# Kernel tuning notes

Measured on AMD Instinct MI355X. Metric: run time of the kernel, lower is better.

The kernel has to match this reference:

```python
import jax, jax.numpy as jnp
import numpy as np

EPS = 1e-5  # BatchNorm eps (torch default)

def _bn(x, mean, var, gamma, beta):
    # eval-mode BatchNorm over the trailing (heads, ch) axes
    return (x - mean) * (gamma / jnp.sqrt(var + EPS)) + beta

def setup_inputs() -> dict:
    key = jax.random.key(0)
    ks = jax.random.split(key, 8)
    B, C, W, H = 16, 256, 64, 64
    heads, k, u, m = 4, 16, 1, 23
    vv = 256
    kh, vh = k // heads, vv // heads
    x = jax.random.normal(ks[0], (B, C, W, H), dtype=jnp.float32)
    q_w = jax.random.normal(ks[1], (heads, kh, C), dtype=jnp.float32) * 0.05
    k_w = jax.random.normal(ks[2], (heads, kh * u, C), dtype=jnp.float32) * 0.05
    v_w = jax.random.normal(ks[3], (heads, vh * u, C), dtype=jnp.float32) * 0.05
    q_gamma = 0.5 + jax.random.uniform(ks[4], (heads, kh), dtype=jnp.float32)
    q_beta = jax.random.normal(ks[5], (heads, kh), dtype=jnp.float32) * 0.1
    q_mean = jnp.zeros((heads, kh), dtype=jnp.float32)
    q_var = jnp.ones((heads, kh), dtype=jnp.float32)
    k_gamma = 0.5 + jax.random.uniform(ks[6], (heads, kh * u), dtype=jnp.float32)
    k_beta = jax.random.normal(ks[7], (heads, kh * u), dtype=jnp.float32) * 0.1
    k_mean = jnp.zeros((heads, kh * u), dtype=jnp.float32)
    k_var = jnp.ones((heads, kh * u), dtype=jnp.float32)
    embedding = jax.random.normal(jax.random.fold_in(key, 99), (kh, heads, u, 1, m, m), dtype=jnp.float32) * 0.05
    return {"x": x, "q_w": q_w, "q_gamma": q_gamma, "q_beta": q_beta, "q_mean": q_mean,
            "q_var": q_var, "k_w": k_w, "k_gamma": k_gamma, "k_beta": k_beta,
            "k_mean": k_mean, "k_var": k_var, "v_w": v_w, "embedding": embedding}

def reference(x, q_w, q_gamma, q_beta, q_mean, q_var, k_w, k_gamma, k_beta, k_mean, k_var, v_w, embedding):
    B, C, W, H = x.shape
    heads, kh, _ = q_w.shape
    u = embedding.shape[2]
    m = embedding.shape[-1]
    vh = v_w.shape[1] // u
    pad = (m - 1) // 2

    # 1x1 conv projections (all heads stacked) -> channels-last
    q = jnp.einsum('bcxy,hkc->bxyhk', x, q_w)                      # [B,W,H,heads,kh]
    q = _bn(q, q_mean, q_var, q_gamma, q_beta)
    kk = jnp.einsum('bcxy,hkc->bxyhk', x, k_w)                     # [B,W,H,heads,kh*u]
    kk = _bn(kk, k_mean, k_var, k_gamma, k_beta)
    # softmax over all spatial positions, per (head, key-channel)
    sm = jax.nn.softmax(kk.reshape(B, W * H, heads, kh * u), axis=1)
    sm = sm.reshape(B, W, H, heads, kh, u)                          # [B,W,H,h,kh,u]
    v = jnp.einsum('bcxy,hvc->bxyhv', x, v_w).reshape(B, W, H, heads, vh, u)

    # content lambda: sum over all spatial positions
    lambda_c = jnp.einsum('bxyhku,bxyhvu->bhkv', sm, v)             # [B,h,kh,vh]
    y_c = jnp.einsum('bxyhk,bhkv->bxyhv', q, lambda_c)              # [B,W,H,h,vh]

    # positional lambda via grouped 2D conv (conv3d kernel depth is 1 -> 2D conv per vh slice)
    v_conv = v.transpose(0, 4, 3, 5, 1, 2).reshape(B * vh, heads * u, W, H)
    w = jnp.squeeze(embedding, axis=3).transpose(1, 0, 2, 3, 4).reshape(heads * kh, u, m, m)
    conv = jax.lax.conv_general_dilated(
        v_conv, w, window_strides=(1, 1), padding=[(pad, pad), (pad, pad)],
        dimension_numbers=('NCHW', 'OIHW', 'NCHW'), feature_group_count=heads)
    # [B*vh, heads*kh, W, H] -> sum over spatial (matches .sum(dim=[1,2]) in source)
    lambda_p = conv.reshape(B, vh, heads, kh, W, H).sum(axis=(4, 5))
    lambda_p = lambda_p.transpose(0, 2, 3, 1)                       # [B,h,kh,vh]
    y_p = jnp.einsum('bxyhk,bhkv->bxyhv', q, lambda_p)

    out = (y_c + y_p).reshape(B, W, H, heads * vh).transpose(0, 3, 1, 2)  # [B,vv,W,H]
    return out
```

## Files before the change

### kernel.cpp

```cpp
#include <hip/hip_runtime.h>
#include <math.h>

#define C_   256
#define WH   4096

typedef _Float16 f16x8 __attribute__((ext_vector_type(8)));
typedef float    f32x4 __attribute__((ext_vector_type(4)));


__global__ __launch_bounds__(256) void wtcomb_kernel(const float* __restrict__ emb,
                                                     const float* __restrict__ pstats,
                                                     float* __restrict__ Wt,
                                                     float* __restrict__ stats)
{
    if (blockIdx.x == 64) {
        int row = threadIdx.x;
        const float* ps = pstats + (size_t)row * 32;
        float M = ps[0];
#pragma unroll
        for (int ch = 1; ch < 16; ++ch) M = fmaxf(M, ps[ch * 2]);
        float S = 0.f;
#pragma unroll
        for (int ch = 0; ch < 16; ++ch) S += ps[ch * 2 + 1] * __expf(ps[ch * 2] - M);
        stats[row * 2 + 0] = M;
        stats[row * 2 + 1] = 1.f / S;
        return;
    }
    int hk = blockIdx.x >> 2, quarter = blockIdx.x & 3;
    int h = hk >> 2, k = hk & 3;
    const float* e = emb + (size_t)(k * 4 + h) * 529;
    __shared__ float colsum[23][64];
    for (int t = threadIdx.x; t < 23 * 64; t += 256) {
        int i = t / 64, q = t % 64;
        int jlo = max(0, q - 52), jhi = min(22, q + 11);
        float s = 0.f;
        for (int j = jlo; j <= jhi; ++j) s += e[i * 23 + j];
        colsum[i][q] = s;
    }
    __syncthreads();
    for (int tt = threadIdx.x; tt < 1024; tt += 256) {
        int t = quarter * 1024 + tt;
        int p = t >> 6, q = t & 63;
        int ilo = max(0, p - 52), ihi = min(22, p + 11);
        float s = 0.f;
        for (int i = ilo; i <= ihi; ++i) s += colsum[i][q];
        Wt[(size_t)hk * WH + t] = s;
    }
}

__global__ __launch_bounds__(512) void proj_kernel(
    const float* __restrict__ x,
    const float* __restrict__ qw, const float* __restrict__ kw,
    const float* __restrict__ qg, const float* __restrict__ qb,
    const float* __restrict__ qm, const float* __restrict__ qv,
    const float* __restrict__ kg, const float* __restrict__ kb,
    const float* __restrict__ km, const float* __restrict__ kv,
    float* __restrict__ qbn, float* __restrict__ kkbn, float* __restrict__ pstats)
{
    int t = threadIdx.x;
    int b = blockIdx.x >> 4, chunk = blockIdx.x & 15;
    int lane = t & 63;
    int og = __builtin_amdgcn_readfirstlane(t >> 6);
    int isK = og >> 2;
    int o4 = (og & 3) * 4;
    int xy = chunk * 256 + lane * 4;

    const float* wsrc = isK ? kw : qw;
    const float* w0 = wsrc + (size_t)(o4 + 0) * 256;
    const float* w1 = wsrc + (size_t)(o4 + 1) * 256;
    const float* w2 = wsrc + (size_t)(o4 + 2) * 256;
    const float* w3 = wsrc + (size_t)(o4 + 3) * 256;

    float4 a0 = {0,0,0,0}, a1 = {0,0,0,0}, a2 = {0,0,0,0}, a3 = {0,0,0,0};
    const float* xb = x + (size_t)b * C_ * WH + xy;
#pragma unroll 8
    for (int c = 0; c < 256; ++c) {
        float4 xv = *(const float4*)(xb + (size_t)c * WH);
        float f0 = w0[c], f1 = w1[c], f2 = w2[c], f3 = w3[c];
        a0.x += xv.x*f0; a0.y += xv.y*f0; a0.z += xv.z*f0; a0.w += xv.w*f0;
        a1.x += xv.x*f1; a1.y += xv.y*f1; a1.z += xv.z*f1; a1.w += xv.w*f1;
        a2.x += xv.x*f2; a2.y += xv.y*f2; a2.z += xv.z*f2; a2.w += xv.w*f2;
        a3.x += xv.x*f3; a3.y += xv.y*f3; a3.z += xv.z*f3; a3.w += xv.w*f3;
    }
    float4 acc4[4] = {a0, a1, a2, a3};

    if (!isK) {
#pragma unroll
        for (int i = 0; i < 4; ++i) {
            int hk = o4 + i;
            float s  = qg[hk] * rsqrtf(qv[hk] + 1e-5f);
            float tq = qb[hk] - qm[hk] * s;
            float4 a = acc4[i], o;
            o.x = a.x * s + tq; o.y = a.y * s + tq;
            o.z = a.z * s + tq; o.w = a.w * s + tq;
            *(float4*)(qbn + ((size_t)b * 16 + hk) * WH + xy) = o;
        }
    } else {
#pragma unroll
        for (int i = 0; i < 4; ++i) {
            int hk = o4 + i;
            float s2 = kg[hk] * rsqrtf(kv[hk] + 1e-5f);
            float tk = kb[hk] - km[hk] * s2;
            float4 a = acc4[i], o;
            o.x = a.x * s2 + tk; o.y = a.y * s2 + tk;
            o.z = a.z * s2 + tk; o.w = a.w * s2 + tk;
            *(float4*)(kkbn + ((size_t)b * 16 + hk) * WH + xy) = o;
            float m = fmaxf(fmaxf(o.x, o.y), fmaxf(o.z, o.w));
#pragma unroll
            for (int off = 32; off; off >>= 1) m = fmaxf(m, __shfl_xor(m, off, 64));
            float e = __expf(o.x - m) + __expf(o.y - m) + __expf(o.z - m) + __expf(o.w - m);
#pragma unroll
            for (int off = 32; off; off >>= 1) e += __shfl_xor(e, off, 64);
            if (lane == 0) {
                float* ps = pstats + ((size_t)(b * 16 + hk) * 16 + chunk) * 2;
                ps[0] = m; ps[1] = e;
            }
        }
    }
}

__global__ __launch_bounds__(512) void ut_kernel(
    const float* __restrict__ x, const float* __restrict__ kkbn,
    const float* __restrict__ stats, const float* __restrict__ Wt,
    float* __restrict__ Mpart)
{
    __shared__ _Float16 xls[256][72];
    __shared__ _Float16 wls[32][72];
    int t = threadIdx.x;
    int b = blockIdx.x >> 4, seg = blockIdx.x & 15;
    int xys0 = seg * 256;
    int lane = t & 63;
    int wid = __builtin_amdgcn_readfirstlane(t >> 6);
    int r16 = lane & 15, g = lane >> 4;
    int n0 = wid * 32;

    int sc = t >> 1, shalf = t & 1;
    int wr = t >> 3, wco = (t & 7) * 8;
    float wm = 0.f, winv = 0.f;
    if (t < 256 && wr < 16) {
        wm   = stats[(b * 16 + wr) * 2 + 0];
        winv = stats[(b * 16 + wr) * 2 + 1];
    }

    f32x4 acc00 = {0.f,0.f,0.f,0.f}, acc01 = {0.f,0.f,0.f,0.f};
    f32x4 acc10 = {0.f,0.f,0.f,0.f}, acc11 = {0.f,0.f,0.f,0.f};

    for (int ch = 0; ch < 4; ++ch) {
        int kbase = xys0 + ch * 64;
        __syncthreads();
        {
            const float* xp = x + ((size_t)b * C_ + sc) * WH + kbase + shalf * 32;
#pragma unroll
            for (int j = 0; j < 4; ++j) {
                float4 u  = *(const float4*)(xp + j * 8);
                float4 u2 = *(const float4*)(xp + j * 8 + 4);
                f16x8 o;
                o[0] = (_Float16)u.x;  o[1] = (_Float16)u.y;
                o[2] = (_Float16)u.z;  o[3] = (_Float16)u.w;
                o[4] = (_Float16)u2.x; o[5] = (_Float16)u2.y;
                o[6] = (_Float16)u2.z; o[7] = (_Float16)u2.w;
                *(f16x8*)&xls[sc][shalf * 32 + j * 8] = o;
            }
        }
        if (t < 256) {
            f16x8 o;
            if (wr < 16) {
                const float* src = kkbn + ((size_t)b * 16 + wr) * WH + kbase + wco;
                float4 u  = *(const float4*)(src);
                float4 u2 = *(const float4*)(src + 4);
                o[0] = (_Float16)(__expf(u.x  - wm) * winv);
                o[1] = (_Float16)(__expf(u.y  - wm) * winv);
                o[2] = (_Float16)(__expf(u.z  - wm) * winv);
                o[3] = (_Float16)(__expf(u.w  - wm) * winv);
                o[4] = (_Float16)(__expf(u2.x - wm) * winv);
                o[5] = (_Float16)(__expf(u2.y - wm) * winv);
                o[6] = (_Float16)(__expf(u2.z - wm) * winv);
                o[7] = (_Float16)(__expf(u2.w - wm) * winv);
            } else {
                const float* src = Wt + (size_t)(wr - 16) * WH + kbase + wco;
                float4 u  = *(const float4*)(src);
                float4 u2 = *(const float4*)(src + 4);
                o[0] = (_Float16)u.x;  o[1] = (_Float16)u.y;
                o[2] = (_Float16)u.z;  o[3] = (_Float16)u.w;
                o[4] = (_Float16)u2.x; o[5] = (_Float16)u2.y;
                o[6] = (_Float16)u2.z; o[7] = (_Float16)u2.w;
            }
            *(f16x8*)&wls[wr][wco] = o;
        }
        __syncthreads();
#pragma unroll
        for (int s = 0; s < 2; ++s) {
            int koff = s * 32 + g * 8;
            f16x8 A0 = *(const f16x8*)&wls[r16     ][koff];
            f16x8 A1 = *(const f16x8*)&wls[16 + r16][koff];
            f16x8 B0 = *(const f16x8*)&xls[n0 + r16     ][koff];
            f16x8 B1 = *(const f16x8*)&xls[n0 + 16 + r16][koff];
            acc00 = __builtin_amdgcn_mfma_f32_16x16x32_f16(A0, B0, acc00, 0, 0, 0);
            acc01 = __builtin_amdgcn_mfma_f32_16x16x32_f16(A0, B1, acc01, 0, 0, 0);
            acc10 = __builtin_amdgcn_mfma_f32_16x16x32_f16(A1, B0, acc10, 0, 0, 0);
            acc11 = __builtin_amdgcn_mfma_f32_16x16x32_f16(A1, B1, acc11, 0, 0, 0);
        }
    }

    float* mp = Mpart + (size_t)(b * 16 + seg) * 8192;
    int colA = n0 + r16, colB = n0 + 16 + r16;
    int row0 = g * 4, row1 = 16 + g * 4;
#pragma unroll
    for (int rr = 0; rr < 4; ++rr) {
        mp[(row0 + rr) * 256 + colA] = acc00[rr];
        mp[(row0 + rr) * 256 + colB] = acc01[rr];
        mp[(row1 + rr) * 256 + colA] = acc10[rr];
        mp[(row1 + rr) * 256 + colB] = acc11[rr];
    }
}

__global__ __launch_bounds__(256) void lam_kernel(
    const float* __restrict__ Mpart, const float* __restrict__ vw,
    float* __restrict__ lam)
{
    __shared__ float msum[256];
    __shared__ float vls[64][68];
    __shared__ float psum[4][64];
    int t = threadIdx.x;
    int b = blockIdx.x >> 4, hk = blockIdx.x & 15, h = hk >> 2;

    {
        const float* mp = Mpart + (size_t)b * 16 * 8192 + t;
        float s = 0.f;
        for (int seg = 0; seg < 16; ++seg) {
            const float* m2 = mp + (size_t)seg * 8192;
            s += m2[hk * 256] + m2[(16 + hk) * 256];
        }
        msum[t] = s;
    }

    int v = t & 63, cq = t >> 6;
    float acc = 0.f;
    const float* vwh = vw + (size_t)h * 64 * 256;
    for (int ch = 0; ch < 4; ++ch) {
        __syncthreads();
#pragma unroll
        for (int k = 0; k < 4; ++k) {
            int e = t + k * 256;
            int vv = e >> 4, c4 = (e & 15) * 4;
            *(float4*)&vls[vv][c4] = *(const float4*)(vwh + (size_t)vv * 256 + ch * 64 + c4);
        }
        __syncthreads();
#pragma unroll
        for (int i4 = 0; i4 < 4; ++i4) {
            float4 a  = *(const float4*)&vls[v][cq * 16 + i4 * 4];
            float4 m4 = *(const float4*)&msum[ch * 64 + cq * 16 + i4 * 4];
            acc += a.x * m4.x + a.y * m4.y + a.z * m4.z + a.w * m4.w;
        }
    }
    psum[cq][v] = acc;
    __syncthreads();
    if (t < 64)
        lam[((size_t)b * 16 + hk) * 64 + t] =
            psum[0][t] + psum[1][t] + psum[2][t] + psum[3][t];
}

__global__ __launch_bounds__(256) void out_kernel(
    const float* __restrict__ qbn, const float* __restrict__ lam,
    float* __restrict__ out)
{
    int t = threadIdx.x;
    int b = blockIdx.x >> 4, s = blockIdx.x & 15;
    int h = s >> 2, qc = s & 3;
    int xy = qc * 1024 + t * 4;
    float4 q0 = *(const float4*)(qbn + ((size_t)b * 16 + h * 4 + 0) * WH + xy);
    float4 q1 = *(const float4*)(qbn + ((size_t)b * 16 + h * 4 + 1) * WH + xy);
    float4 q2 = *(const float4*)(qbn + ((size_t)b * 16 + h * 4 + 2) * WH + xy);
    float4 q3 = *(const float4*)(qbn + ((size_t)b * 16 + h * 4 + 3) * WH + xy);
    const float* lb = lam + (size_t)b * 1024 + (size_t)h * 256;
    float* ob = out + ((size_t)b * 256 + (size_t)h * 64) * WH + xy;
#pragma unroll 8
    for (int v = 0; v < 64; ++v) {
        float l0 = lb[v], l1 = lb[64 + v], l2 = lb[128 + v], l3 = lb[192 + v];
        float4 o;
        o.x = q0.x*l0 + q1.x*l1 + q2.x*l2 + q3.x*l3;
        o.y = q0.y*l0 + q1.y*l1 + q2.y*l2 + q3.y*l3;
        o.z = q0.z*l0 + q1.z*l1 + q2.z*l2 + q3.z*l3;
        o.w = q0.w*l0 + q1.w*l1 + q2.w*l2 + q3.w*l3;
        *(float4*)(ob + (size_t)v * WH) = o;
    }
}

extern "C" void kernel_launch(void* const* d_in, const int* in_sizes, int n_in,
                              void* d_out, int out_size, void* d_ws, size_t ws_size,
                              hipStream_t stream)
{
    const float* x   = (const float*)d_in[0];
    const float* qw  = (const float*)d_in[1];
    const float* qg  = (const float*)d_in[2];
    const float* qb  = (const float*)d_in[3];
    const float* qm  = (const float*)d_in[4];
    const float* qv  = (const float*)d_in[5];
    const float* kw  = (const float*)d_in[6];
    const float* kg  = (const float*)d_in[7];
    const float* kb  = (const float*)d_in[8];
    const float* km  = (const float*)d_in[9];
    const float* kv  = (const float*)d_in[10];
    const float* vw  = (const float*)d_in[11];
    const float* emb = (const float*)d_in[12];

    float* ws    = (float*)d_ws;
    float* qbn   = ws;
    float* kkbn  = ws + 1048576;
    float* stats = ws + 2097152;
    float* Wt    = ws + 2097664;
    float* Mpart = ws + 2163200;
    float* pstats = Mpart;
    float* lam   = ws + 4260352;
    float* out   = (float*)d_out;

    hipLaunchKernelGGL(proj_kernel,  dim3(256), dim3(512), 0, stream,
                       x, qw, kw, qg, qb, qm, qv, kg, kb, km, kv, qbn, kkbn, pstats);
    hipLaunchKernelGGL(wtcomb_kernel, dim3(65), dim3(256), 0, stream, emb, pstats, Wt, stats);
    hipLaunchKernelGGL(ut_kernel,    dim3(256), dim3(512), 0, stream,
                       x, kkbn, stats, Wt, Mpart);
    hipLaunchKernelGGL(lam_kernel,   dim3(256), dim3(256), 0, stream, Mpart, vw, lam);
    hipLaunchKernelGGL(out_kernel,   dim3(256), dim3(256), 0, stream, qbn, lam, out);
}
```

Before: 86.67 us.

## Fold wtcomb into proj and ut kernels, double ut_kernel grid

Drops the separate wtcomb kernel. The positional-weight (Wt) computation moves into 64 extra blocks of proj_kernel, and the softmax stat reduction moves into each ut_kernel block through shared memory. ut_kernel now splits each batch into 32 spatial segments of 128 instead of 16 of 256, giving 512 blocks, and lam_kernel sums 32 partials. This removes one launch and its serialization and raises parallelism in ut_kernel, at the cost of twice the Mpart partial traffic and a redundant stat reduction in every block.

```diff
diff --git a/kernel.cpp b/kernel.cpp
--- a/kernel.cpp
+++ b/kernel.cpp
@@ -7,46 +7,6 @@
 typedef _Float16 f16x8 __attribute__((ext_vector_type(8)));
 typedef float    f32x4 __attribute__((ext_vector_type(4)));
 
-
-__global__ __launch_bounds__(256) void wtcomb_kernel(const float* __restrict__ emb,
-                                                     const float* __restrict__ pstats,
-                                                     float* __restrict__ Wt,
-                                                     float* __restrict__ stats)
-{
-    if (blockIdx.x == 64) {
-        int row = threadIdx.x;
-        const float* ps = pstats + (size_t)row * 32;
-        float M = ps[0];
-#pragma unroll
-        for (int ch = 1; ch < 16; ++ch) M = fmaxf(M, ps[ch * 2]);
-        float S = 0.f;
-#pragma unroll
-        for (int ch = 0; ch < 16; ++ch) S += ps[ch * 2 + 1] * __expf(ps[ch * 2] - M);
-        stats[row * 2 + 0] = M;
-        stats[row * 2 + 1] = 1.f / S;
-        return;
-    }
-    int hk = blockIdx.x >> 2, quarter = blockIdx.x & 3;
-    int h = hk >> 2, k = hk & 3;
-    const float* e = emb + (size_t)(k * 4 + h) * 529;
-    __shared__ float colsum[23][64];
-    for (int t = threadIdx.x; t < 23 * 64; t += 256) {
-        int i = t / 64, q = t % 64;
-        int jlo = max(0, q - 52), jhi = min(22, q + 11);
-        float s = 0.f;
-        for (int j = jlo; j <= jhi; ++j) s += e[i * 23 + j];
-        colsum[i][q] = s;
-    }
-    __syncthreads();
-    for (int tt = threadIdx.x; tt < 1024; tt += 256) {
-        int t = quarter * 1024 + tt;
-        int p = t >> 6, q = t & 63;
-        int ilo = max(0, p - 52), ihi = min(22, p + 11);
-        float s = 0.f;
-        for (int i = ilo; i <= ihi; ++i) s += colsum[i][q];
-        Wt[(size_t)hk * WH + t] = s;
-    }
-}
 
 __global__ __launch_bounds__(512) void proj_kernel(
     const float* __restrict__ x,
@@ -55,8 +15,35 @@
     const float* __restrict__ qm, const float* __restrict__ qv,
     const float* __restrict__ kg, const float* __restrict__ kb,
     const float* __restrict__ km, const float* __restrict__ kv,
-    float* __restrict__ qbn, float* __restrict__ kkbn, float* __restrict__ pstats)
-{
+    const float* __restrict__ emb,
+    float* __restrict__ qbn, float* __restrict__ kkbn,
+    float* __restrict__ pstats, float* __restrict__ Wt)
+{
+    if (blockIdx.x >= 256) {
+        int wb = blockIdx.x - 256;
+        int hk = wb >> 2, quarter = wb & 3;
+        int h = hk >> 2, k = hk & 3;
+        const float* e = emb + (size_t)(k * 4 + h) * 529;
+        __shared__ float colsum[23][64];
+        for (int t2 = threadIdx.x; t2 < 23 * 64; t2 += 512) {
+            int i = t2 / 64, q = t2 % 64;
+            int jlo = max(0, q - 52), jhi = min(22, q + 11);
+            float s = 0.f;
+            for (int j = jlo; j <= jhi; ++j) s += e[i * 23 + j];
+            colsum[i][q] = s;
+        }
+        __syncthreads();
+        for (int tt = threadIdx.x; tt < 1024; tt += 512) {
+            int t2 = quarter * 1024 + tt;
+            int p = t2 >> 6, q = t2 & 63;
+            int ilo = max(0, p - 52), ihi = min(22, p + 11);
+            float s = 0.f;
+            for (int i = ilo; i <= ihi; ++i) s += colsum[i][q];
+            Wt[(size_t)hk * WH + t2] = s;
+        }
+        return;
+    }
+
     int t = threadIdx.x;
     int b = blockIdx.x >> 4, chunk = blockIdx.x & 15;
     int lane = t & 63;
@@ -121,31 +108,39 @@
 
 __global__ __launch_bounds__(512) void ut_kernel(
     const float* __restrict__ x, const float* __restrict__ kkbn,
-    const float* __restrict__ stats, const float* __restrict__ Wt,
+    const float* __restrict__ pstats, const float* __restrict__ Wt,
     float* __restrict__ Mpart)
 {
     __shared__ _Float16 xls[256][72];
     __shared__ _Float16 wls[32][72];
+    __shared__ float st[32];
     int t = threadIdx.x;
-    int b = blockIdx.x >> 4, seg = blockIdx.x & 15;
-    int xys0 = seg * 256;
+    int b = blockIdx.x >> 5, s5 = blockIdx.x & 31;
+    int xys0 = s5 * 128;
     int lane = t & 63;
     int wid = __builtin_amdgcn_readfirstlane(t >> 6);
     int r16 = lane & 15, g = lane >> 4;
     int n0 = wid * 32;
 
+    if (t < 16) {
+        const float* ps = pstats + (size_t)(b * 16 + t) * 32;
+        float M = ps[0];
+#pragma unroll
+        for (int ch = 1; ch < 16; ++ch) M = fmaxf(M, ps[ch * 2]);
+        float S = 0.f;
+#pragma unroll
+        for (int ch = 0; ch < 16; ++ch) S += ps[ch * 2 + 1] * __expf(ps[ch * 2] - M);
+        st[2 * t]     = M;
+        st[2 * t + 1] = 1.f / S;
+    }
+
     int sc = t >> 1, shalf = t & 1;
     int wr = t >> 3, wco = (t & 7) * 8;
-    float wm = 0.f, winv = 0.f;
-    if (t < 256 && wr < 16) {
-        wm   = stats[(b * 16 + wr) * 2 + 0];
-        winv = stats[(b * 16 + wr) * 2 + 1];
-    }
 
     f32x4 acc00 = {0.f,0.f,0.f,0.f}, acc01 = {0.f,0.f,0.f,0.f};
     f32x4 acc10 = {0.f,0.f,0.f,0.f}, acc11 = {0.f,0.f,0.f,0.f};
 
-    for (int ch = 0; ch < 4; ++ch) {
+    for (int ch = 0; ch < 2; ++ch) {
         int kbase = xys0 + ch * 64;
         __syncthreads();
         {
@@ -165,6 +160,8 @@
         if (t < 256) {
             f16x8 o;
             if (wr < 16) {
+                float wm   = st[2 * wr];
+                float winv = st[2 * wr + 1];
                 const float* src = kkbn + ((size_t)b * 16 + wr) * WH + kbase + wco;
                 float4 u  = *(const float4*)(src);
                 float4 u2 = *(const float4*)(src + 4);
@@ -202,7 +199,7 @@
         }
     }
 
-    float* mp = Mpart + (size_t)(b * 16 + seg) * 8192;
+    float* mp = Mpart + (size_t)(b * 32 + s5) * 8192;
     int colA = n0 + r16, colB = n0 + 16 + r16;
     int row0 = g * 4, row1 = 16 + g * 4;
 #pragma unroll
@@ -225,9 +222,9 @@
     int b = blockIdx.x >> 4, hk = blockIdx.x & 15, h = hk >> 2;
 
     {
-        const float* mp = Mpart + (size_t)b * 16 * 8192 + t;
+        const float* mp = Mpart + (size_t)b * 32 * 8192 + t;
         float s = 0.f;
-        for (int seg = 0; seg < 16; ++seg) {
+        for (int seg = 0; seg < 32; ++seg) {
             const float* m2 = mp + (size_t)seg * 8192;
             s += m2[hk * 256] + m2[(16 + hk) * 256];
         }
@@ -304,21 +301,20 @@
     const float* vw  = (const float*)d_in[11];
     const float* emb = (const float*)d_in[12];
 
-    float* ws    = (float*)d_ws;
-    float* qbn   = ws;
-    float* kkbn  = ws + 1048576;
-    float* stats = ws + 2097152;
-    float* Wt    = ws + 2097664;
-    float* Mpart = ws + 2163200;
-    float* pstats = Mpart;
-    float* lam   = ws + 4260352;
-    float* out   = (float*)d_out;
-
-    hipLaunchKernelGGL(proj_kernel,  dim3(256), dim3(512), 0, stream,
-                       x, qw, kw, qg, qb, qm, qv, kg, kb, km, kv, qbn, kkbn, pstats);
-    hipLaunchKernelGGL(wtcomb_kernel, dim3(65), dim3(256), 0, stream, emb, pstats, Wt, stats);
-    hipLaunchKernelGGL(ut_kernel,    dim3(256), dim3(512), 0, stream,
-                       x, kkbn, stats, Wt, Mpart);
+    float* ws     = (float*)d_ws;
+    float* qbn    = ws;
+    float* kkbn   = ws + 1048576;
+    float* pstats = ws + 2097152;
+    float* Wt     = ws + 2105344;
+    float* Mpart  = ws + 2170880;
+    float* lam    = ws + 6365184;
+    float* out    = (float*)d_out;
+
+    hipLaunchKernelGGL(proj_kernel,  dim3(320), dim3(512), 0, stream,
+                       x, qw, kw, qg, qb, qm, qv, kg, kb, km, kv, emb,
+                       qbn, kkbn, pstats, Wt);
+    hipLaunchKernelGGL(ut_kernel,    dim3(512), dim3(512), 0, stream,
+                       x, kkbn, pstats, Wt, Mpart);
     hipLaunchKernelGGL(lam_kernel,   dim3(256), dim3(256), 0, stream, Mpart, vw, lam);
     hipLaunchKernelGGL(out_kernel,   dim3(256), dim3(256), 0, stream, qbn, lam, out);
 }
```

New measurement: 74.48 us. -14.1%, faster.
